# Optimization experiments

Measured on AMD Instinct MI355X. Metric: run time of the kernel, lower is better.

## Reference

```python
import jax, jax.numpy as jnp
import numpy as np

N_NODES = 100000
N_EDGES = 1600000
IN_DIM = 128
HID = 32
HEADS = 4
NUM_CLASS = 2


def setup_inputs() -> dict:
    key = jax.random.key(0)
    ks = jax.random.split(key, 10)
    x = jax.random.normal(ks[0], (N_NODES, IN_DIM), dtype=jnp.float32)
    edge_index = jax.random.randint(ks[1], (2, N_EDGES), 0, N_NODES, dtype=jnp.int64)
    s_in = 1.0 / np.sqrt(IN_DIM)
    s_h = 1.0 / np.sqrt(HEADS * HID)
    return {
        "x": x,
        "edge_index": edge_index,
        "W1": jax.random.normal(ks[2], (HEADS * HID, IN_DIM), dtype=jnp.float32) * s_in,
        "att_src1": jax.random.normal(ks[3], (HEADS, HID), dtype=jnp.float32) * s_in,
        "att_dst1": jax.random.normal(ks[4], (HEADS, HID), dtype=jnp.float32) * s_in,
        "b1": jnp.zeros((HEADS * HID,), dtype=jnp.float32),
        "W2": jax.random.normal(ks[5], (NUM_CLASS, HEADS * HID), dtype=jnp.float32) * s_h,
        "att_src2": jax.random.normal(ks[6], (1, NUM_CLASS), dtype=jnp.float32) * s_h,
        "att_dst2": jax.random.normal(ks[7], (1, NUM_CLASS), dtype=jnp.float32) * s_h,
        "b2": jnp.zeros((NUM_CLASS,), dtype=jnp.float32),
    }


def gat_conv(x, src, dst, W, att_src, att_dst, b, n):
    """PyG-style GATConv (self-loops already included in src/dst)."""
    H, C = att_src.shape
    h = (x @ W.T).reshape(n, H, C)                      # [N,H,C]
    a_s = jnp.einsum('nhc,hc->nh', h, att_src)           # [N,H]
    a_d = jnp.einsum('nhc,hc->nh', h, att_dst)           # [N,H]
    e = jax.nn.leaky_relu(a_s[src] + a_d[dst], 0.2)      # [E,H]
    m = jax.ops.segment_max(e, dst, num_segments=n)      # per-dst max
    m = jnp.where(jnp.isfinite(m), m, 0.0)
    ex = jnp.exp(e - m[dst])
    denom = jax.ops.segment_sum(ex, dst, num_segments=n)
    alpha = ex / (denom[dst] + 1e-16)                    # segment softmax
    out = jax.ops.segment_sum(h[src] * alpha[..., None], dst, num_segments=n)
    return out.reshape(n, H * C) + b


def reference(x, edge_index, W1, att_src1, att_dst1, b1, W2, att_src2, att_dst2, b2):
    n = x.shape[0]
    loops = jnp.arange(n, dtype=edge_index.dtype)
    ei = jnp.concatenate([edge_index, jnp.stack([loops, loops])], axis=1)
    src, dst = ei[0], ei[1]
    h = gat_conv(x, src, dst, W1, att_src1, att_dst1, b1, n)
    h = jax.nn.leaky_relu(h, 0.01)  # F.leaky_relu default slope
    # F.dropout with p=0.0 -> identity
    out = gat_conv(h, src, dst, W2, att_src2, att_dst2, b2, n)
    return jax.nn.log_softmax(out, axis=1)
```

## Files before the change

### kernel.cpp

```cpp
#include <hip/hip_runtime.h>

#define NN 100000
#define NE 1600000
#define NTOT (NN + NE)
#define NB 782
#define ACHUNK 4096
#define BCAP 3072

typedef __attribute__((ext_vector_type(8))) short bf16x8;
typedef __attribute__((ext_vector_type(4))) float f32x4;

static __device__ __forceinline__ float blo(unsigned int u) {
  union { unsigned int i; float f; } v; v.i = u << 16; return v.f;
}
static __device__ __forceinline__ float bhi(unsigned int u) {
  union { unsigned int i; float f; } v; v.i = u & 0xffff0000u; return v.f;
}
static __device__ __forceinline__ unsigned short f2bf(float f) {
  union { float f; unsigned int i; } v; v.f = f;
  unsigned int i = v.i;
  i += 0x7fffu + ((i >> 16) & 1u);
  return (unsigned short)(i >> 16);
}

__global__ void k_zero(int* __restrict__ bucketCnt) {
  int i = threadIdx.x;
  if (i < NB) bucketCnt[i] = 0;
}

__global__ __launch_bounds__(256) void kb_hist(const int* __restrict__ ei,
                                               int* __restrict__ bucketCnt) {
  __shared__ int h[NB];
  int tid = threadIdx.x;
  for (int i = tid; i < NB; i += 256) h[i] = 0;
  __syncthreads();
  for (int i = blockIdx.x * 256 + tid; i < NE; i += gridDim.x * 256)
    atomicAdd(&h[ei[NE + i] >> 7], 1);
  __syncthreads();
  for (int i = tid; i < NB; i += 256)
    if (h[i]) atomicAdd(&bucketCnt[i], h[i]);
}

__global__ void kb_scan(const int* __restrict__ bucketCnt, int* __restrict__ pairOffset,
                        int* __restrict__ bucketCursor) {
  int lane = threadIdx.x;
  int c[13];
  int run = 0;
  int idx0 = lane * 13;
#pragma unroll
  for (int k = 0; k < 13; ++k) {
    int idx = idx0 + k;
    int v = (idx < NB) ? bucketCnt[idx] : 0;
    c[k] = run;
    run += v;
  }
  int x = run;
#pragma unroll
  for (int d = 1; d < 64; d <<= 1) {
    int y = __shfl_up(x, d, 64);
    if (lane >= d) x += y;
  }
  int laneoff = x - run;
#pragma unroll
  for (int k = 0; k < 13; ++k) {
    int idx = idx0 + k;
    if (idx <= NB) {
      int e = laneoff + c[k];
      pairOffset[idx] = e;
      if (idx < NB) bucketCursor[idx] = e;
    }
  }
}

__global__ __launch_bounds__(512) void kb_scatA(const int* __restrict__ ei,
                                                int* __restrict__ bucketCursor,
                                                int* __restrict__ pair) {
  __shared__ int lcnt[NB + 1];
  __shared__ int gbase[NB];
  __shared__ int lcur[NB];
  __shared__ int stage[ACHUNK];
  int tid = threadIdx.x;
  int e0 = blockIdx.x * ACHUNK;
  int n = min(ACHUNK, NE - e0);
  for (int i = tid; i <= NB; i += 512) lcnt[i] = 0;
  __syncthreads();
  for (int i = tid; i < n; i += 512) atomicAdd(&lcnt[ei[NE + e0 + i] >> 7], 1);
  __syncthreads();
  if (tid < 64) {
    int c[13];
    int run = 0;
    int idx0 = tid * 13;
#pragma unroll
    for (int k = 0; k < 13; ++k) {
      int idx = idx0 + k;
      int v = (idx < NB) ? lcnt[idx] : 0;
      c[k] = run;
      run += v;
    }
    int x = run;
#pragma unroll
    for (int d = 1; d < 64; d <<= 1) {
      int y = __shfl_up(x, d, 64);
      if (tid >= d) x += y;
    }
    int laneoff = x - run;
#pragma unroll
    for (int k = 0; k < 13; ++k) {
      int idx = idx0 + k;
      if (idx <= NB) lcnt[idx] = laneoff + c[k];
    }
  }
  __syncthreads();
  for (int b = tid; b < NB; b += 512) {
    int base = lcnt[b], cnt = lcnt[b + 1] - base;
    gbase[b] = cnt ? atomicAdd(&bucketCursor[b], cnt) : 0;
    lcur[b] = base;
  }
  __syncthreads();
  for (int i = tid; i < n; i += 512) {
    int s = ei[e0 + i], d = ei[NE + e0 + i];
    int b = d >> 7;
    int p = atomicAdd(&lcur[b], 1);
    stage[p] = (s << 7) | (d & 127);
  }
  __syncthreads();
  for (int b = tid; b < NB; b += 512) {
    int base = lcnt[b], cnt = lcnt[b + 1] - base, g = gbase[b];
    for (int k = 0; k < cnt; ++k) pair[g + k] = stage[base + k];
  }
}

__global__ __launch_bounds__(256) void kb_binB(const int* __restrict__ pair,
                                               const int* __restrict__ pairOffset,
                                               int* __restrict__ rowptr,
                                               int* __restrict__ col) {
  __shared__ int cnt[128];
  __shared__ int cur[128];
  __shared__ int stage[BCAP];
  int tid = threadIdx.x;
  int b = blockIdx.x;
  int dbase = b << 7;
  int nd = min(128, NN - dbase);
  int pbeg = pairOffset[b], m = pairOffset[b + 1] - pbeg;
  int cbase = pbeg + dbase;
  if (tid < 128) cnt[tid] = 0;
  __syncthreads();
  for (int i = tid; i < m; i += 256) atomicAdd(&cnt[pair[pbeg + i] & 127], 1);
  __syncthreads();
  if (tid < 64) {
    int i0 = 2 * tid, i1 = 2 * tid + 1;
    int v0 = cnt[i0] + (i0 < nd ? 1 : 0);
    int v1 = cnt[i1] + (i1 < nd ? 1 : 0);
    int run = v0 + v1;
    int x = run;
#pragma unroll
    for (int d = 1; d < 64; d <<= 1) {
      int y = __shfl_up(x, d, 64);
      if (tid >= d) x += y;
    }
    int e0 = x - run;
    int e1 = e0 + v0;
    if (i0 < nd) { rowptr[dbase + i0] = cbase + e0; stage[e0] = dbase + i0; cur[i0] = e0 + 1; }
    else cur[i0] = e0;
    if (i1 < nd) { rowptr[dbase + i1] = cbase + e1; stage[e1] = dbase + i1; cur[i1] = e1 + 1; }
    else cur[i1] = e1;
  }
  if (b == NB - 1 && tid == 0) rowptr[NN] = NTOT;
  __syncthreads();
  for (int i = tid; i < m; i += 256) {
    int p = pair[pbeg + i];
    int pos = atomicAdd(&cur[p & 127], 1);
    stage[pos] = p >> 7;
  }
  __syncthreads();
  int tot = m + nd;
  for (int i = tid; i < tot; i += 256) col[cbase + i] = stage[i];
}

__global__ void k_cvtW(const float* __restrict__ W1, unsigned short* __restrict__ Wh,
                       unsigned short* __restrict__ Wl) {
  int i = blockIdx.x * 256 + threadIdx.x;
  if (i < 128 * 128) {
    float v = W1[i];
    unsigned short h = f2bf(v);
    Wh[i] = h;
    Wl[i] = f2bf(v - blo((unsigned int)h));
  }
}

__global__ __launch_bounds__(256) void k_gemm1(
    const float* __restrict__ x, const unsigned short* __restrict__ Wh,
    const unsigned short* __restrict__ Wl, const float* __restrict__ asrc,
    const float* __restrict__ adst, unsigned short* __restrict__ h1b,
    float4* __restrict__ as1, float4* __restrict__ ad1) {
  __shared__ unsigned short hstage[4][16][128];
  int wid = threadIdx.x >> 6, lane = threadIdx.x & 63;
  int tile = blockIdx.x * 4 + wid;
  if (tile >= NN / 16) tile = NN / 16 - 1;
  int r16 = lane & 15, quad = lane >> 4;
  const float* xrow = x + (size_t)(tile * 16 + r16) * 128 + quad * 8;
  bf16x8 ah[4], al[4];
#pragma unroll
  for (int c = 0; c < 4; ++c)
#pragma unroll
    for (int j = 0; j < 8; ++j) {
      float v = xrow[c * 32 + j];
      unsigned short h = f2bf(v);
      ah[c][j] = (short)h;
      al[c][j] = (short)f2bf(v - blo((unsigned int)h));
    }
  float asp[4][4], adp[4][4];
#pragma unroll
  for (int h = 0; h < 4; ++h)
#pragma unroll
    for (int r = 0; r < 4; ++r) { asp[h][r] = 0.f; adp[h][r] = 0.f; }
#pragma unroll
  for (int ot = 0; ot < 8; ++ot) {
    const bf16x8* whrow = (const bf16x8*)(Wh + (size_t)(ot * 16 + r16) * 128);
    const bf16x8* wlrow = (const bf16x8*)(Wl + (size_t)(ot * 16 + r16) * 128);
    f32x4 acc = {0.f, 0.f, 0.f, 0.f};
#pragma unroll
    for (int c = 0; c < 4; ++c) {
      bf16x8 wh = whrow[c * 4 + quad];
      bf16x8 wl = wlrow[c * 4 + quad];
      acc = __builtin_amdgcn_mfma_f32_16x16x32_bf16(ah[c], wh, acc, 0, 0, 0);
      acc = __builtin_amdgcn_mfma_f32_16x16x32_bf16(ah[c], wl, acc, 0, 0, 0);
      acc = __builtin_amdgcn_mfma_f32_16x16x32_bf16(al[c], wh, acc, 0, 0, 0);
    }
    float sa = asrc[ot * 16 + r16], da = adst[ot * 16 + r16];
    const int hh = ot >> 1;
#pragma unroll
    for (int r = 0; r < 4; ++r) {
      asp[hh][r] += acc[r] * sa;
      adp[hh][r] += acc[r] * da;
    }
    unsigned short* st = &hstage[wid][quad * 4][ot * 16 + r16];
    st[0] = f2bf(acc[0]); st[128] = f2bf(acc[1]);
    st[256] = f2bf(acc[2]); st[384] = f2bf(acc[3]);
  }
#pragma unroll
  for (int h = 0; h < 4; ++h)
#pragma unroll
    for (int r = 0; r < 4; ++r) {
      float v = asp[h][r];
      v += __shfl_xor(v, 1, 64); v += __shfl_xor(v, 2, 64);
      v += __shfl_xor(v, 4, 64); v += __shfl_xor(v, 8, 64);
      asp[h][r] = v;
      float w = adp[h][r];
      w += __shfl_xor(w, 1, 64); w += __shfl_xor(w, 2, 64);
      w += __shfl_xor(w, 4, 64); w += __shfl_xor(w, 8, 64);
      adp[h][r] = w;
    }
#pragma unroll
  for (int r = 0; r < 4; ++r) {
    if (r16 == r) {
      int node = tile * 16 + quad * 4 + r;
      as1[node] = make_float4(asp[0][r], asp[1][r], asp[2][r], asp[3][r]);
      ad1[node] = make_float4(adp[0][r], adp[1][r], adp[2][r], adp[3][r]);
    }
  }
  __syncthreads();
  const uint4* src = (const uint4*)&hstage[wid][0][0];
  uint4* dst = (uint4*)(h1b + (size_t)tile * 16 * 128);
#pragma unroll
  for (int i = 0; i < 4; ++i) dst[i * 64 + lane] = src[i * 64 + lane];
}

__global__ __launch_bounds__(256, 8) void k_agg1(
    const unsigned short* __restrict__ h1b, const float* __restrict__ as1,
    const float* __restrict__ ad1, const int* __restrict__ rowptr,
    const int* __restrict__ col, const float* __restrict__ b1,
    const float* __restrict__ W2, const float* __restrict__ asrc2,
    const float* __restrict__ adst2, float4* __restrict__ node2) {
  int wid = threadIdx.x >> 6, lane = threadIdx.x & 63;
  int grp = lane >> 4, l16 = lane & 15;
  int node = blockIdx.x * 16 + wid * 4 + grp;
  int head = l16 >> 2;
  float ad = ad1[node * 4 + head];
  int beg = rowptr[node], deg = rowptr[node + 1] - beg;
  const uint4* h1q = (const uint4*)h1b;
  float acc[8] = {0.f, 0.f, 0.f, 0.f, 0.f, 0.f, 0.f, 0.f};
  float wsum = 0.f;
  int j = 0;
  while (__ballot(j < deg)) {
    bool a[4]; int s[4];
#pragma unroll
    for (int k = 0; k < 4; ++k) {
      a[k] = (j + k) < deg;
      s[k] = a[k] ? col[beg + j + k] : 0;
    }
    float e[4]; uint4 u[4];
#pragma unroll
    for (int k = 0; k < 4; ++k) e[k] = as1[s[k] * 4 + head] + ad;
#pragma unroll
    for (int k = 0; k < 4; ++k) u[k] = h1q[(size_t)s[k] * 16 + l16];
#pragma unroll
    for (int k = 0; k < 4; ++k) {
      float t = e[k];
      t = (t < 0.f) ? 0.2f * t : t;
      float w = a[k] ? __expf(fminf(t, 80.f)) : 0.f;
      wsum += w;
      acc[0] += w * blo(u[k].x); acc[1] += w * bhi(u[k].x);
      acc[2] += w * blo(u[k].y); acc[3] += w * bhi(u[k].y);
      acc[4] += w * blo(u[k].z); acc[5] += w * bhi(u[k].z);
      acc[6] += w * blo(u[k].w); acc[7] += w * bhi(u[k].w);
    }
    j += 4;
  }
  float inv = 1.f / (wsum + 1e-16f);
  int cb = l16 * 8;
  float h[8];
#pragma unroll
  for (int t = 0; t < 8; ++t) {
    float v = acc[t] * inv + b1[cb + t];
    h[t] = (v < 0.f) ? 0.01f * v : v;
  }
  float p0 = 0.f, p1 = 0.f;
#pragma unroll
  for (int t = 0; t < 8; ++t) {
    p0 += h[t] * W2[cb + t];
    p1 += h[t] * W2[128 + cb + t];
  }
  p0 += __shfl_xor(p0, 1, 64); p0 += __shfl_xor(p0, 2, 64);
  p0 += __shfl_xor(p0, 4, 64); p0 += __shfl_xor(p0, 8, 64);
  p1 += __shfl_xor(p1, 1, 64); p1 += __shfl_xor(p1, 2, 64);
  p1 += __shfl_xor(p1, 4, 64); p1 += __shfl_xor(p1, 8, 64);
  if (l16 == 0) {
    float as2 = p0 * asrc2[0] + p1 * asrc2[1];
    float ad2 = p0 * adst2[0] + p1 * adst2[1];
    node2[node] = make_float4(p0, p1, as2, ad2);
  }
}

__global__ void k_agg2(const float4* __restrict__ node2, const int* __restrict__ rowptr,
                       const int* __restrict__ col, const float* __restrict__ b2,
                       float2* __restrict__ out) {
  int t = blockIdx.x * 256 + threadIdx.x;
  int node = t >> 2, sub = t & 3;
  if (node >= NN) return;
  float ad2 = node2[node].w;
  int beg = rowptr[node], end = rowptr[node + 1];
  float den = 0.f, a0 = 0.f, a1 = 0.f;
  for (int j = beg + sub; j < end; j += 4) {
    int s = col[j];
    float4 sv = node2[s];
    float e = sv.z + ad2;
    e = (e < 0.f) ? 0.2f * e : e;
    float w = __expf(fminf(e, 80.f));
    den += w;
    a0 += w * sv.x;
    a1 += w * sv.y;
  }
#pragma unroll
  for (int d = 1; d < 4; d <<= 1) {
    den += __shfl_xor(den, d, 64);
    a0 += __shfl_xor(a0, d, 64);
    a1 += __shfl_xor(a1, d, 64);
  }
  if (sub == 0) {
    float inv = 1.f / (den + 1e-16f);
    float o0 = a0 * inv + b2[0];
    float o1 = a1 * inv + b2[1];
    float m = fmaxf(o0, o1);
    float lse = m + __logf(__expf(o0 - m) + __expf(o1 - m));
    out[node] = make_float2(o0 - lse, o1 - lse);
  }
}

extern "C" void kernel_launch(void* const* d_in, const int* in_sizes, int n_in,
                              void* d_out, int out_size, void* d_ws, size_t ws_size,
                              hipStream_t stream) {
  const float* x     = (const float*)d_in[0];
  const int*   ei    = (const int*)d_in[1];
  const float* W1    = (const float*)d_in[2];
  const float* asrc1 = (const float*)d_in[3];
  const float* adst1 = (const float*)d_in[4];
  const float* b1    = (const float*)d_in[5];
  const float* W2    = (const float*)d_in[6];
  const float* asrc2 = (const float*)d_in[7];
  const float* adst2 = (const float*)d_in[8];
  const float* b2    = (const float*)d_in[9];
  float2* out = (float2*)d_out;

  int* rowptr       = (int*)d_ws;
  int* col          = rowptr + 100352;
  int* pair         = col + 1700096;
  int* bucketCnt    = pair + 1600000;
  int* pairOffset   = bucketCnt + 1024;
  int* bucketCursor = pairOffset + 1024;
  unsigned short* h1b = (unsigned short*)(bucketCursor + 1024);
  float*  as1  = (float*)(h1b + (size_t)NN * 128);
  float*  ad1  = as1 + NN * 4;
  float4* node2 = (float4*)(ad1 + NN * 4);
  unsigned short* W1h = (unsigned short*)(node2 + NN);
  unsigned short* W1l = W1h + 16384;

  k_zero<<<1, 1024, 0, stream>>>(bucketCnt);
  kb_hist<<<782, 256, 0, stream>>>(ei, bucketCnt);
  kb_scan<<<1, 64, 0, stream>>>(bucketCnt, pairOffset, bucketCursor);
  kb_scatA<<<(NE + ACHUNK - 1) / ACHUNK, 512, 0, stream>>>(ei, bucketCursor, pair);
  kb_binB<<<NB, 256, 0, stream>>>(pair, pairOffset, rowptr, col);
  k_cvtW<<<64, 256, 0, stream>>>(W1, W1h, W1l);
  k_gemm1<<<(NN / 16 + 3) / 4, 256, 0, stream>>>(x, W1h, W1l, asrc1, adst1, h1b,
                                                 (float4*)as1, (float4*)ad1);
  k_agg1<<<NN / 16, 256, 0, stream>>>(h1b, as1, ad1, rowptr, col, b1, W2, asrc2, adst2, node2);
  k_agg2<<<(NN * 4 + 255) / 256, 256, 0, stream>>>(node2, rowptr, col, b2, out);
}
```

Before: 290.4 us.

## Replace atomic bucket cursors with per-chunk count matrix and column scan

The bucket-sort histogram now writes per-chunk bucket counts to a matrix. A new column-scan kernel computes exclusive prefix offsets per bucket across chunks, so the scatter kernel derives global bases directly instead of using global atomics on bucket cursors. This makes edge placement deterministic and drops the zeroing kernel, at the cost of an extra launch and a matrix round-trip. Separately, the layer-1 aggregation unrolls the neighbor loop from 4 to 8 gathers per iteration, with launch bounds lowered from 8 to 6 blocks to leave room for the extra registers.

```diff
diff --git a/kernel.cpp b/kernel.cpp
--- a/kernel.cpp
+++ b/kernel.cpp
@@ -5,6 +5,7 @@
 #define NTOT (NN + NE)
 #define NB 782
 #define ACHUNK 4096
+#define NCH 391
 #define BCAP 3072
 
 typedef __attribute__((ext_vector_type(8))) short bf16x8;
@@ -23,26 +24,39 @@
   return (unsigned short)(i >> 16);
 }
 
-__global__ void k_zero(int* __restrict__ bucketCnt) {
-  int i = threadIdx.x;
-  if (i < NB) bucketCnt[i] = 0;
-}
-
-__global__ __launch_bounds__(256) void kb_hist(const int* __restrict__ ei,
-                                               int* __restrict__ bucketCnt) {
+__global__ __launch_bounds__(512) void kb_hist(const int* __restrict__ ei,
+                                               int* __restrict__ cntMat) {
   __shared__ int h[NB];
-  int tid = threadIdx.x;
-  for (int i = tid; i < NB; i += 256) h[i] = 0;
-  __syncthreads();
-  for (int i = blockIdx.x * 256 + tid; i < NE; i += gridDim.x * 256)
-    atomicAdd(&h[ei[NE + i] >> 7], 1);
-  __syncthreads();
-  for (int i = tid; i < NB; i += 256)
-    if (h[i]) atomicAdd(&bucketCnt[i], h[i]);
-}
-
-__global__ void kb_scan(const int* __restrict__ bucketCnt, int* __restrict__ pairOffset,
-                        int* __restrict__ bucketCursor) {
+  int tid = threadIdx.x, blk = blockIdx.x;
+  int e0 = blk * ACHUNK;
+  int n = min(ACHUNK, NE - e0);
+  for (int i = tid; i < NB; i += 512) h[i] = 0;
+  __syncthreads();
+  for (int i = tid; i < n; i += 512) atomicAdd(&h[ei[NE + e0 + i] >> 7], 1);
+  __syncthreads();
+  for (int i = tid; i < NB; i += 512) cntMat[blk * NB + i] = h[i];
+}
+
+__global__ void kb_colscan(int* __restrict__ cntMat, int* __restrict__ bucketCnt) {
+  int b = blockIdx.x;
+  int lane = threadIdx.x;
+  int carry = 0;
+  for (int base = 0; base < NCH; base += 64) {
+    int idx = base + lane;
+    int v = (idx < NCH) ? cntMat[idx * NB + b] : 0;
+    int x = v;
+#pragma unroll
+    for (int d = 1; d < 64; d <<= 1) {
+      int y = __shfl_up(x, d, 64);
+      if (lane >= d) x += y;
+    }
+    if (idx < NCH) cntMat[idx * NB + b] = carry + x - v;
+    carry += __shfl(x, 63, 64);
+  }
+  if (lane == 0) bucketCnt[b] = carry;
+}
+
+__global__ void kb_scan(const int* __restrict__ bucketCnt, int* __restrict__ pairOffset) {
   int lane = threadIdx.x;
   int c[13];
   int run = 0;
@@ -64,23 +78,20 @@
 #pragma unroll
   for (int k = 0; k < 13; ++k) {
     int idx = idx0 + k;
-    if (idx <= NB) {
-      int e = laneoff + c[k];
-      pairOffset[idx] = e;
-      if (idx < NB) bucketCursor[idx] = e;
-    }
+    if (idx <= NB) pairOffset[idx] = laneoff + c[k];
   }
 }
 
 __global__ __launch_bounds__(512) void kb_scatA(const int* __restrict__ ei,
-                                                int* __restrict__ bucketCursor,
+                                                const int* __restrict__ pairOffset,
+                                                const int* __restrict__ cntMat,
                                                 int* __restrict__ pair) {
   __shared__ int lcnt[NB + 1];
   __shared__ int gbase[NB];
   __shared__ int lcur[NB];
   __shared__ int stage[ACHUNK];
-  int tid = threadIdx.x;
-  int e0 = blockIdx.x * ACHUNK;
+  int tid = threadIdx.x, blk = blockIdx.x;
+  int e0 = blk * ACHUNK;
   int n = min(ACHUNK, NE - e0);
   for (int i = tid; i <= NB; i += 512) lcnt[i] = 0;
   __syncthreads();
@@ -112,9 +123,8 @@
   }
   __syncthreads();
   for (int b = tid; b < NB; b += 512) {
-    int base = lcnt[b], cnt = lcnt[b + 1] - base;
-    gbase[b] = cnt ? atomicAdd(&bucketCursor[b], cnt) : 0;
-    lcur[b] = base;
+    gbase[b] = pairOffset[b] + cntMat[blk * NB + b];
+    lcur[b] = lcnt[b];
   }
   __syncthreads();
   for (int i = tid; i < n; i += 512) {
@@ -266,7 +276,7 @@
   for (int i = 0; i < 4; ++i) dst[i * 64 + lane] = src[i * 64 + lane];
 }
 
-__global__ __launch_bounds__(256, 8) void k_agg1(
+__global__ __launch_bounds__(256, 6) void k_agg1(
     const unsigned short* __restrict__ h1b, const float* __restrict__ as1,
     const float* __restrict__ ad1, const int* __restrict__ rowptr,
     const int* __restrict__ col, const float* __restrict__ b1,
@@ -283,19 +293,19 @@
   float wsum = 0.f;
   int j = 0;
   while (__ballot(j < deg)) {
-    bool a[4]; int s[4];
-#pragma unroll
-    for (int k = 0; k < 4; ++k) {
+    bool a[8]; int s[8];
+#pragma unroll
+    for (int k = 0; k < 8; ++k) {
       a[k] = (j + k) < deg;
       s[k] = a[k] ? col[beg + j + k] : 0;
     }
-    float e[4]; uint4 u[4];
-#pragma unroll
-    for (int k = 0; k < 4; ++k) e[k] = as1[s[k] * 4 + head] + ad;
-#pragma unroll
-    for (int k = 0; k < 4; ++k) u[k] = h1q[(size_t)s[k] * 16 + l16];
-#pragma unroll
-    for (int k = 0; k < 4; ++k) {
+    float e[8]; uint4 u[8];
+#pragma unroll
+    for (int k = 0; k < 8; ++k) e[k] = as1[s[k] * 4 + head] + ad;
+#pragma unroll
+    for (int k = 0; k < 8; ++k) u[k] = h1q[(size_t)s[k] * 16 + l16];
+#pragma unroll
+    for (int k = 0; k < 8; ++k) {
       float t = e[k];
       t = (t < 0.f) ? 0.2f * t : t;
       float w = a[k] ? __expf(fminf(t, 80.f)) : 0.f;
@@ -305,7 +315,7 @@
       acc[4] += w * blo(u[k].z); acc[5] += w * bhi(u[k].z);
       acc[6] += w * blo(u[k].w); acc[7] += w * bhi(u[k].w);
     }
-    j += 4;
+    j += 8;
   }
   float inv = 1.f / (wsum + 1e-16f);
   int cb = l16 * 8;
@@ -382,23 +392,23 @@
   const float* b2    = (const float*)d_in[9];
   float2* out = (float2*)d_out;
 
-  int* rowptr       = (int*)d_ws;
-  int* col          = rowptr + 100352;
-  int* pair         = col + 1700096;
-  int* bucketCnt    = pair + 1600000;
-  int* pairOffset   = bucketCnt + 1024;
-  int* bucketCursor = pairOffset + 1024;
-  unsigned short* h1b = (unsigned short*)(bucketCursor + 1024);
+  int* rowptr     = (int*)d_ws;
+  int* col        = rowptr + 100352;
+  int* pair       = col + 1700096;
+  int* cntMat     = pair + 1600000;
+  int* bucketCnt  = cntMat + 305792;
+  int* pairOffset = bucketCnt + 1024;
+  unsigned short* h1b = (unsigned short*)(pairOffset + 1024);
   float*  as1  = (float*)(h1b + (size_t)NN * 128);
   float*  ad1  = as1 + NN * 4;
   float4* node2 = (float4*)(ad1 + NN * 4);
   unsigned short* W1h = (unsigned short*)(node2 + NN);
   unsigned short* W1l = W1h + 16384;
 
-  k_zero<<<1, 1024, 0, stream>>>(bucketCnt);
-  kb_hist<<<782, 256, 0, stream>>>(ei, bucketCnt);
-  kb_scan<<<1, 64, 0, stream>>>(bucketCnt, pairOffset, bucketCursor);
-  kb_scatA<<<(NE + ACHUNK - 1) / ACHUNK, 512, 0, stream>>>(ei, bucketCursor, pair);
+  kb_hist<<<NCH, 512, 0, stream>>>(ei, cntMat);
+  kb_colscan<<<NB, 64, 0, stream>>>(cntMat, bucketCnt);
+  kb_scan<<<1, 64, 0, stream>>>(bucketCnt, pairOffset);
+  kb_scatA<<<NCH, 512, 0, stream>>>(ei, pairOffset, cntMat, pair);
   kb_binB<<<NB, 256, 0, stream>>>(pair, pairOffset, rowptr, col);
   k_cvtW<<<64, 256, 0, stream>>>(W1, W1h, W1l);
   k_gemm1<<<(NN / 16 + 3) / 4, 256, 0, stream>>>(x, W1h, W1l, asrc1, adst1, h1b,
```

Result: faster. 275.6 us (-5.1%).
